# Optimization experiments

Hardware: AMD Instinct MI355X
Metric: run time of the kernel (lower is better)

The kernel has to match this reference:

```python
import jax, jax.numpy as jnp
import numpy as np

B, T, V, H = 256, 2048, 128, 64  # batch, seq_len, vocab/input_size, hidden_size


def setup_inputs() -> dict:
    key = jax.random.key(0)
    ks = jax.random.split(key, 11)
    s = 0.1  # weight scale
    d = jnp.float32
    return {
        "x": jax.random.normal(ks[0], (B, T, V), dtype=d),
        "W_f": jax.random.normal(ks[1], (V + H, H), dtype=d) * s,
        "b_f": jax.random.normal(ks[2], (H,), dtype=d) * s,
        "W_if": jax.random.normal(ks[3], (V + H, H), dtype=d) * s,
        "b_if": jax.random.normal(ks[4], (H,), dtype=d) * s,
        "W_ic": jax.random.normal(ks[5], (V + H, H), dtype=d) * s,
        "b_ic": jax.random.normal(ks[6], (H,), dtype=d) * s,
        "W_o": jax.random.normal(ks[7], (V + H, H), dtype=d) * s,
        "b_o": jax.random.normal(ks[8], (H,), dtype=d) * s,
        "W_out": jax.random.normal(ks[9], (H, V), dtype=d) * s,
        "b_out": jax.random.normal(ks[10], (V,), dtype=d) * s,
    }


def reference(x, W_f, b_f, W_if, b_if, W_ic, b_ic, W_o, b_o, W_out, b_out):
    # Manual LSTM cell from the source, stepped over time with lax.scan.
    # Per step (faithful to forward()+getOut()):
    #   s = concat(x_t, h);  f = sigmoid(s@W_f+b_f);  c = c*f
    #   add = tanh(s@W_ic+b_ic); af = sigmoid(s@W_if+b_if); c = c + add*af
    #   o = sigmoid(s@W_o+b_o);  h = tanh(c)*o
    #   out = softmax(h@W_out+b_out)
    b, t = x.shape[0], x.shape[1]
    h0 = jnp.zeros((b, W_f.shape[1]), dtype=x.dtype)
    c0 = jnp.zeros_like(h0)

    def step(carry, x_t):
        h, c = carry
        s = jnp.concatenate([x_t, h], axis=1)          # [B, V+H]
        f = jax.nn.sigmoid(s @ W_f + b_f)
        add = jnp.tanh(s @ W_ic + b_ic)
        af = jax.nn.sigmoid(s @ W_if + b_if)
        c = c * f + add * af
        o = jax.nn.sigmoid(s @ W_o + b_o)
        h = jnp.tanh(c) * o
        out = jax.nn.softmax(h @ W_out + b_out, axis=-1)  # [B, V]
        return (h, c), out

    (_, _), outs = jax.lax.scan(step, (h0, c0), jnp.swapaxes(x, 0, 1))
    return jnp.swapaxes(outs, 0, 1)  # [B, T, V]
```

## Files before the change

kernel.cpp:

```cpp
#include <hip/hip_runtime.h>
#include <cstdint>
#include <cstddef>

#define BB 256
#define TT 2048
#define VV 128
#define HH 64

typedef __attribute__((ext_vector_type(8))) short short8;
typedef __attribute__((ext_vector_type(4))) float f32x4;
typedef __attribute__((ext_vector_type(2))) float f32x2;

__device__ __forceinline__ float frcp(float x){ return __builtin_amdgcn_rcpf(x); }
__device__ __forceinline__ float sigm(float x){ return frcp(1.f + __expf(-x)); }
__device__ __forceinline__ float tanh_f(float x){ return 1.f - 2.f*frcp(1.f + __expf(2.f*x)); }

__device__ __forceinline__ void bar_lds(){
  asm volatile("s_waitcnt lgkmcnt(0)" ::: "memory");
  __builtin_amdgcn_s_barrier();
  __builtin_amdgcn_sched_barrier(0);
}

__device__ __forceinline__ void gload16(const void* g, void* l){
  __builtin_amdgcn_global_load_lds(
      (const __attribute__((address_space(1))) void*)g,
      (__attribute__((address_space(3))) void*)l, 16, 0, 0);
}

__device__ __forceinline__ unsigned short bf16hi(float x){
  unsigned u = __float_as_uint(x);
  return (unsigned short)((u + 0x7fffu + ((u>>16)&1u)) >> 16);
}
__device__ __forceinline__ void splitpack(const float* v8, short8& hi, short8& lo){
  #pragma unroll
  for (int j=0;j<8;++j){
    unsigned short h = bf16hi(v8[j]);
    float fh = __uint_as_float(((unsigned)h)<<16);
    unsigned short lw = bf16hi(v8[j] - fh);
    hi[j] = (short)h; lo[j] = (short)lw;
  }
}

__device__ __forceinline__ float qsum(float v){
  int t1 = __builtin_amdgcn_update_dpp(0, __float_as_int(v), 0xB1, 0xF, 0xF, true);
  v += __int_as_float(t1);
  int t2 = __builtin_amdgcn_update_dpp(0, __float_as_int(v), 0x4E, 0xF, 0xF, true);
  v += __int_as_float(t2);
  return v;
}

template<int CTRL>
__device__ __forceinline__ float dppmov(float v){
  return __int_as_float(__builtin_amdgcn_update_dpp(0, __float_as_int(v), CTRL, 0xF, 0xF, true));
}

__device__ __forceinline__ void pkfma(f32x2& acc, f32x2 a, f32x2 b){
  asm volatile("v_pk_fma_f32 %0, %1, %2, %0" : "+v"(acc) : "v"(a), "v"(b));
}

__global__ __launch_bounds__(256) void conv_w_k(
  const float* __restrict__ Wf, const float* __restrict__ Wi,
  const float* __restrict__ Wc, const float* __restrict__ Wo,
  const float* __restrict__ Wout,
  unsigned short* __restrict__ W4h, unsigned short* __restrict__ W4l,
  unsigned short* __restrict__ WOh, unsigned short* __restrict__ WOl)
{
  const int idx = blockIdx.x*256 + threadIdx.x;
  if (idx < 32768){
    const int j = idx&7, l=(idx>>3)&63, kk=(idx>>9)&3, nt=idx>>11;
    const int k = kk*32 + (l>>4)*8 + j;
    const int n = nt*16 + (l&15);
    const int g = n&3, colw = n>>2;
    const float* Ws = (g==0)?Wf:((g==1)?Wi:((g==2)?Wc:Wo));
    const float v = Ws[k*HH + colw];
    const unsigned short h = bf16hi(v);
    const float fh = __uint_as_float(((unsigned)h)<<16);
    W4h[idx] = h; W4l[idx] = bf16hi(v - fh);
  }
  if (idx < 8192){
    const int j = idx&7, l=(idx>>3)&63, kk=(idx>>9)&1, jt=idx>>10;
    const int k = kk*32 + (l>>4)*8 + j;
    const int jc = jt*16 + (l&15);
    const float v = Wout[k*VV + jc];
    const unsigned short h = bf16hi(v);
    const float fh = __uint_as_float(((unsigned)h)<<16);
    WOh[idx] = h; WOl[idx] = bf16hi(v - fh);
  }
}

__global__ __launch_bounds__(512,1) void pre_gemm_k(
  const float* __restrict__ x, const unsigned short* __restrict__ W4h,
  const unsigned short* __restrict__ W4l, float* __restrict__ PRE)
{
  __shared__ __align__(16) unsigned short XFh[16384];
  __shared__ __align__(16) unsigned short XFl[16384];
  const int tid = threadIdx.x, wv = tid>>6, l = tid&63, b = blockIdx.x;

  short8 Bh[2][4], Bl[2][4];
  #pragma unroll
  for (int ntl=0; ntl<2; ++ntl){
    const int nt = wv*2 + ntl;
    #pragma unroll
    for (int kk=0; kk<4; ++kk){
      Bh[ntl][kk] = *(const short8*)(W4h + ((nt*4+kk)*64 + l)*8);
      Bl[ntl][kk] = *(const short8*)(W4l + ((nt*4+kk)*64 + l)*8);
    }
  }

  #pragma unroll 1
  for (int mt=0; mt<16; ++mt){
    const size_t base_row = (size_t)b*TT + mt*128;
    #pragma unroll
    for (int i=0;i<4;++i){
      const int G = tid*4+i;
      const int lf = G&63, kk=(G>>6)&3, m8=G>>8;
      const float* src = x + (base_row + m8*16 + (lf&15))*VV + kk*32 + (lf>>4)*8;
      const f32x4 u = *(const f32x4*)src;
      const f32x4 v = *(const f32x4*)(src+4);
      float tmp[8] = {u[0],u[1],u[2],u[3], v[0],v[1],v[2],v[3]};
      short8 hi, lo; splitpack(tmp, hi, lo);
      *(short8*)&XFh[(size_t)G*8] = hi;
      *(short8*)&XFl[(size_t)G*8] = lo;
    }
    bar_lds();
    for (int m8=0; m8<8; ++m8){
      short8 Ah[4], Al[4];
      #pragma unroll
      for (int kk=0;kk<4;++kk){
        Ah[kk] = *(const short8*)&XFh[((m8*4+kk)*64 + l)*8];
        Al[kk] = *(const short8*)&XFl[((m8*4+kk)*64 + l)*8];
      }
      #pragma unroll
      for (int ntl=0; ntl<2; ++ntl){
        f32x4 acc = {0.f,0.f,0.f,0.f};
        #pragma unroll
        for (int kk=0;kk<4;++kk){
          acc = __builtin_amdgcn_mfma_f32_16x16x32_bf16(Al[kk], Bh[ntl][kk], acc, 0,0,0);
          acc = __builtin_amdgcn_mfma_f32_16x16x32_bf16(Ah[kk], Bl[ntl][kk], acc, 0,0,0);
          acc = __builtin_amdgcn_mfma_f32_16x16x32_bf16(Ah[kk], Bh[ntl][kk], acc, 0,0,0);
        }
        const int nt = wv*2 + ntl;
        float* dst = PRE + (base_row + m8*16 + (l>>4)*4)*256 + nt*16 + (l&15);
        #pragma unroll
        for (int r=0;r<4;++r) dst[(size_t)r*256] = acc[r];
      }
    }
    bar_lds();
  }
}

__global__ __launch_bounds__(256,1) void recur4_k(
  const float* __restrict__ W_f, const float* __restrict__ b_f,
  const float* __restrict__ W_if, const float* __restrict__ b_if,
  const float* __restrict__ W_ic, const float* __restrict__ b_ic,
  const float* __restrict__ W_o,  const float* __restrict__ b_o,
  const float* __restrict__ PRE,  float* __restrict__ H)
{
  __shared__ __align__(16) float ring[16*256];
  __shared__ __align__(16) float hring[32*HH];
  const int tid=threadIdx.x, wv=tid>>6, l=tid&63, b=blockIdx.x;
  const int col = wv*16 + (l>>2), q = l&3;
  const bool qb0 = (l&1)!=0, qb1 = (l&2)!=0;

  f32x2 wf2[8], wi2[8], wc2[8], wo2[8];
  #pragma unroll
  for (int m=0;m<8;++m){
    const size_t k0 = (size_t)(VV + q*16 + 2*m)*HH + col;
    wf2[m] = f32x2{W_f [k0], W_f [k0+HH]};
    wi2[m] = f32x2{W_if[k0], W_if[k0+HH]};
    wc2[m] = f32x2{W_ic[k0], W_ic[k0+HH]};
    wo2[m] = f32x2{W_o [k0], W_o [k0+HH]};
  }
  const float bq  = ((q==0)?b_f:(q==1)?b_if:(q==2)?b_ic:b_o)[col];
  const float sgn = (q==2)? 2.f : -1.f;
  const float aA  = (q==2)? -2.f : 1.f;
  const float aB  = (q==2)? 1.f : 0.f;

  const float* PREb = PRE + (size_t)b*TT*256;
  float* Hb = H + (size_t)b*TT*HH;
  const f32x4* ring4  = (const f32x4*)ring;
  const f32x4* hring4 = (const f32x4*)hring;

  if (tid < HH) hring[31*HH + tid] = 0.f;

  if (wv==0){
    asm volatile("s_waitcnt vmcnt(0)" ::: "memory");
    #pragma unroll 1
    for (int s=0;s<15;++s) gload16(PREb + s*256 + l*4, &ring[s*256]);
    asm volatile("s_waitcnt vmcnt(14)" ::: "memory");
  }
  bar_lds();

  float c_ = 0.f;
  #pragma unroll 1
  for (int t=0;t<TT;++t){
    if (wv==1 && t>0 && (t&15)==0){
      #pragma unroll
      for (int i=0;i<4;++i){
        const int rt = t-16 + i*4 + (l>>4);
        const f32x4 v = hring4[(rt&31)*16 + (l&15)];
        *(f32x4*)(Hb + (size_t)rt*HH + (l&15)*4) = v;
      }
    }
    const int rprev = (t+31)&31;
    const f32x4 pre = ring4[(t&15)*64 + col];
    const f32x4* hp = &hring4[rprev*16 + q*4];
    const f32x4 h0 = hp[0], h1 = hp[1], h2 = hp[2], h3 = hp[3];
    f32x2 a0={0.f,0.f}, a1={0.f,0.f}, a2={0.f,0.f}, a3={0.f,0.f};
    {
      const f32x2 p0 = f32x2{h0[0],h0[1]}, p1 = f32x2{h0[2],h0[3]};
      const f32x2 p2 = f32x2{h1[0],h1[1]}, p3 = f32x2{h1[2],h1[3]};
      const f32x2 p4 = f32x2{h2[0],h2[1]}, p5 = f32x2{h2[2],h2[3]};
      const f32x2 p6 = f32x2{h3[0],h3[1]}, p7 = f32x2{h3[2],h3[3]};
      pkfma(a0,p0,wf2[0]); pkfma(a0,p1,wf2[1]); pkfma(a0,p2,wf2[2]); pkfma(a0,p3,wf2[3]);
      pkfma(a0,p4,wf2[4]); pkfma(a0,p5,wf2[5]); pkfma(a0,p6,wf2[6]); pkfma(a0,p7,wf2[7]);
      pkfma(a1,p0,wi2[0]); pkfma(a1,p1,wi2[1]); pkfma(a1,p2,wi2[2]); pkfma(a1,p3,wi2[3]);
      pkfma(a1,p4,wi2[4]); pkfma(a1,p5,wi2[5]); pkfma(a1,p6,wi2[6]); pkfma(a1,p7,wi2[7]);
      pkfma(a2,p0,wc2[0]); pkfma(a2,p1,wc2[1]); pkfma(a2,p2,wc2[2]); pkfma(a2,p3,wc2[3]);
      pkfma(a2,p4,wc2[4]); pkfma(a2,p5,wc2[5]); pkfma(a2,p6,wc2[6]); pkfma(a2,p7,wc2[7]);
      pkfma(a3,p0,wo2[0]); pkfma(a3,p1,wo2[1]); pkfma(a3,p2,wo2[2]); pkfma(a3,p3,wo2[3]);
      pkfma(a3,p4,wo2[4]); pkfma(a3,p5,wo2[5]); pkfma(a3,p6,wo2[6]); pkfma(a3,p7,wo2[7]);
    }
    const float a0s = a0[0]+a0[1];
    const float a1s = a1[0]+a1[1];
    const float a2s = a2[0]+a2[1];
    const float a3s = a3[0]+a3[1];
    float tA = qb0 ? a1s : a0s;
    float tB = qb0 ? a0s : a1s;
    tA += dppmov<0xB1>(tB);
    float tC = qb0 ? a3s : a2s;
    float tD = qb0 ? a2s : a3s;
    tC += dppmov<0xB1>(tD);
    float r  = qb1 ? tC : tA;
    float rr = qb1 ? tA : tC;
    r += dppmov<0x4E>(rr);
    const float pm01 = qb0 ? pre[1] : pre[0];
    const float pm23 = qb0 ? pre[3] : pre[2];
    const float pq   = qb1 ? pm23 : pm01;
    const float xx  = r + pq + bq;
    const float e   = __expf(sgn*xx);
    const float rc  = frcp(1.f + e);
    const float act = fmaf(aA, rc, aB);
    const float f_  = dppmov<0x00>(act);
    const float af  = dppmov<0x55>(act);
    const float ad  = dppmov<0xAA>(act);
    const float o_  = dppmov<0xFF>(act);
    c_ = c_*f_ + ad*af;
    const float hv = tanh_f(c_) * o_;
    if (q==0) hring[(t&31)*HH + col] = hv;
    if (wv==0){
      gload16(PREb + (size_t)((t+15)&(TT-1))*256 + l*4, &ring[((t+15)&15)*256]);
      asm volatile("s_waitcnt vmcnt(14)" ::: "memory");
    }
    bar_lds();
  }
  if (wv==1){
    #pragma unroll
    for (int i=0;i<4;++i){
      const int rt = TT-16 + i*4 + (l>>4);
      const f32x4 v = hring4[(rt&31)*16 + (l&15)];
      *(f32x4*)(Hb + (size_t)rt*HH + (l&15)*4) = v;
    }
  }
}

__global__ __launch_bounds__(512,1) void logit_k(
  const float* __restrict__ H, const unsigned short* __restrict__ WOh,
  const unsigned short* __restrict__ WOl, const float* __restrict__ b_out,
  float* __restrict__ out)
{
  const int tid=threadIdx.x, wv=tid>>6, l=tid&63, b=blockIdx.x;
  short8 Bh[8][2], Bl[8][2];
  #pragma unroll
  for (int jt=0;jt<8;++jt){
    #pragma unroll
    for (int kk=0;kk<2;++kk){
      Bh[jt][kk] = *(const short8*)(WOh + ((jt*2+kk)*64 + l)*8);
      Bl[jt][kk] = *(const short8*)(WOl + ((jt*2+kk)*64 + l)*8);
    }
  }
  float bj[8];
  #pragma unroll
  for (int jt=0;jt<8;++jt) bj[jt] = b_out[jt*16 + (l&15)];

  #pragma unroll 1
  for (int mt=0; mt<16; ++mt){
    const size_t row0 = (size_t)b*TT + mt*128 + wv*16;
    const float* hbase = H + (row0 + (l&15))*HH;
    short8 Ah[2], Al[2];
    #pragma unroll
    for (int kk=0;kk<2;++kk){
      const float* s = hbase + kk*32 + (l>>4)*8;
      const f32x4 u = *(const f32x4*)s;
      const f32x4 v = *(const f32x4*)(s+4);
      float tmp[8] = {u[0],u[1],u[2],u[3], v[0],v[1],v[2],v[3]};
      splitpack(tmp, Ah[kk], Al[kk]);
    }
    f32x4 acc[8];
    #pragma unroll
    for (int jt=0;jt<8;++jt){
      f32x4 a = {0.f,0.f,0.f,0.f};
      #pragma unroll
      for (int kk=0;kk<2;++kk){
        a = __builtin_amdgcn_mfma_f32_16x16x32_bf16(Al[kk], Bh[jt][kk], a, 0,0,0);
        a = __builtin_amdgcn_mfma_f32_16x16x32_bf16(Ah[kk], Bl[jt][kk], a, 0,0,0);
        a = __builtin_amdgcn_mfma_f32_16x16x32_bf16(Ah[kk], Bh[jt][kk], a, 0,0,0);
      }
      acc[jt] = a;
    }
    #pragma unroll
    for (int r=0;r<4;++r){
      float z[8];
      #pragma unroll
      for (int jt=0;jt<8;++jt) z[jt] = acc[jt][r] + bj[jt];
      float mx = z[0];
      #pragma unroll
      for (int jt=1;jt<8;++jt) mx = fmaxf(mx, z[jt]);
      mx = fmaxf(mx, __shfl_xor(mx,1));
      mx = fmaxf(mx, __shfl_xor(mx,2));
      mx = fmaxf(mx, __shfl_xor(mx,4));
      mx = fmaxf(mx, __shfl_xor(mx,8));
      float sum = 0.f;
      #pragma unroll
      for (int jt=0;jt<8;++jt){ z[jt] = __expf(z[jt]-mx); sum += z[jt]; }
      sum += __shfl_xor(sum,1);
      sum += __shfl_xor(sum,2);
      sum += __shfl_xor(sum,4);
      sum += __shfl_xor(sum,8);
      const float rs = frcp(sum);
      float* op = out + (row0 + (l>>4)*4 + r)*VV + (l&15);
      #pragma unroll
      for (int jt=0;jt<8;++jt) op[jt*16] = z[jt]*rs;
    }
  }
}

#define XA_IDX(buf,kk,q,s) ((buf)*2048 + (((kk)*4+(q))*16+(s))*8)
#define HA_IDX(buf,kk,q,s) ((buf)*1024 + (((kk)*4+(q))*16+(s))*8)
#define NBF 128

__device__ __forceinline__ void gload16f(const float* g, float* l){
  __builtin_amdgcn_global_load_lds(
      (const __attribute__((address_space(1))) void*)g,
      (__attribute__((address_space(3))) void*)l, 16, 0, 0);
}

__global__ __launch_bounds__(512, 1) void fused_fb_k(
  const float* __restrict__ x,
  const float* __restrict__ W_f,  const float* __restrict__ b_f,
  const float* __restrict__ W_if, const float* __restrict__ b_if,
  const float* __restrict__ W_ic, const float* __restrict__ b_ic,
  const float* __restrict__ W_o,  const float* __restrict__ b_o,
  const float* __restrict__ W_out,const float* __restrict__ b_out,
  float* __restrict__ out)
{
  __shared__ __align__(16) float XR[4*16*VV];
  __shared__ __align__(16) short XAh[2*2048];
  __shared__ __align__(16) short XAl[2*2048];
  __shared__ __align__(16) float PRE[32*256];
  __shared__ __align__(16) short HAh[2*1024];
  __shared__ __align__(16) short HAl[2*1024];
  __shared__ __align__(16) float HR[32*HH];

  const int tid = threadIdx.x;
  const int wv  = tid >> 6;
  const int l   = tid & 63;
  const int row = blockIdx.x;
  const float* xrow = x   + (size_t)row*TT*VV;
  float*       orow = out + (size_t)row*TT*VV;

  if (wv < 4) {
    const int col = (wv&3)*16 + (l>>2);
    const int q   = l&3;
    float wh0[16], wh1[16], wh2[16], wh3[16];
    #pragma unroll
    for (int m=0;m<16;++m){
      const size_t kidx = (size_t)(VV + q*16 + m)*HH + col;
      wh0[m]=W_f[kidx]; wh1[m]=W_if[kidx]; wh2[m]=W_ic[kidx]; wh3[m]=W_o[kidx];
    }
    const float b0=b_f[col], b1=b_if[col], b2=b_ic[col], b3=b_o[col];
    if (tid < HH) HR[31*HH + tid] = 0.f;
    bar_lds(); bar_lds(); bar_lds();
    float c = 0.f;
    #pragma unroll 1
    for (int t=0; t<TT; ++t){
      const f32x4* hp = (const f32x4*)&HR[((t+31)&31)*HH + q*16];
      const f32x4 pre4 = *(const f32x4*)&PRE[(t&31)*256 + col*4];
      float d0=0.f,d1=0.f,d2=0.f,d3=0.f;
      #pragma unroll
      for (int m=0;m<4;++m){
        const f32x4 hv = hp[m];
        #pragma unroll
        for (int e=0;e<4;++e){
          const float s = hv[e];
          d0 = fmaf(s, wh0[m*4+e], d0);
          d1 = fmaf(s, wh1[m*4+e], d1);
          d2 = fmaf(s, wh2[m*4+e], d2);
          d3 = fmaf(s, wh3[m*4+e], d3);
        }
      }
      d0 = qsum(d0); d1 = qsum(d1); d2 = qsum(d2); d3 = qsum(d3);
      const float f  = sigm(d0 + pre4[0] + b0);
      const float fi = sigm(d1 + pre4[1] + b1);
      const float ci = tanh_f(d2 + pre4[2] + b2);
      const float o  = sigm(d3 + pre4[3] + b3);
      c = c*f + ci*fi;
      const float hv2 = tanh_f(c) * o;
      if (q==0) HR[(t&31)*HH + col] = hv2;
      bar_lds();
    }
    bar_lds();
  } else {
    const int pv = wv - 4;
    const int pt = pv*64 + l;
    short8 Bh[4][4], Bl[4][4];
    #pragma unroll
    for (int ntl=0; ntl<4; ++ntl){
      const int n = (pv*4+ntl)*16 + (l&15);
      const int g = n&3, colw = n>>2;
      const float* Ws = (g==0)?W_f:((g==1)?W_if:((g==2)?W_ic:W_o));
      #pragma unroll
      for (int kk=0;kk<4;++kk){
        float tmp[8];
        #pragma unroll
        for (int j=0;j<8;++j) tmp[j] = Ws[(size_t)(kk*32+(l>>4)*8+j)*HH + colw];
        splitpack(tmp, Bh[ntl][kk], Bl[ntl][kk]);
      }
    }
    short8 Lh[2][2], Ll[2][2];
    #pragma unroll
    for (int jt=0; jt<2; ++jt){
      const int j = (pv*2+jt)*16 + (l&15);
      #pragma unroll
      for (int kk=0;kk<2;++kk){
        float tmp[8];
        #pragma unroll
        for (int jj=0;jj<8;++jj) tmp[jj] = W_out[(size_t)(kk*32+(l>>4)*8+jj)*VV + j];
        splitpack(tmp, Lh[jt][kk], Ll[jt][kk]);
      }
    }
    auto GLOAD = [&](int bb){
      #pragma unroll
      for (int i=0;i<2;++i){
        const float* src = xrow + (size_t)bb*16*VV + pv*512 + i*256 + l*4;
        float* dst = &XR[(bb&3)*2048 + pv*512 + i*256];
        gload16f(src, dst);
      }
    };
    auto CONV = [&](int bb){
      if (pt < 256){
        const int buf=bb&1, kk=pt>>6, qq=(pt>>4)&3, s=pt&15;
        const float* src = &XR[(bb&3)*2048 + s*VV + kk*32 + qq*8];
        float tmp[8];
        #pragma unroll
        for (int j=0;j<8;++j) tmp[j] = src[j];
        short8 hi, lo; splitpack(tmp, hi, lo);
        *(short8*)&XAh[XA_IDX(buf,kk,qq,s)] = hi;
        *(short8*)&XAl[XA_IDX(buf,kk,qq,s)] = lo;
      }
    };
    auto PREB = [&](int bb){
      const int buf = bb&1;
      short8 Ah[4], Al[4];
      #pragma unroll
      for (int kk=0;kk<4;++kk){
        Ah[kk] = *(const short8*)&XAh[XA_IDX(buf,kk,(l>>4),(l&15))];
        Al[kk] = *(const short8*)&XAl[XA_IDX(buf,kk,(l>>4),(l&15))];
      }
      #pragma unroll
      for (int ntl=0; ntl<4; ++ntl){
        f32x4 acc = {0.f,0.f,0.f,0.f};
        #pragma unroll
        for (int kk=0;kk<4;++kk){
          acc = __builtin_amdgcn_mfma_f32_16x16x32_bf16(Al[kk], Bh[ntl][kk], acc, 0,0,0);
          acc = __builtin_amdgcn_mfma_f32_16x16x32_bf16(Ah[kk], Bl[ntl][kk], acc, 0,0,0);
          acc = __builtin_amdgcn_mfma_f32_16x16x32_bf16(Ah[kk], Bh[ntl][kk], acc, 0,0,0);
        }
        const int n  = (pv*4+ntl)*16 + (l&15);
        const int s0 = buf*16 + (l>>4)*4;
        #pragma unroll
        for (int r=0;r<4;++r) PRE[(s0+r)*256 + n] = acc[r];
      }
    };
    auto LOGB = [&](int bb){
      const int buf = bb&1;
      short8 Ah[2], Al[2];
      #pragma unroll
      for (int kk=0;kk<2;++kk){
        Ah[kk] = *(const short8*)&HAh[HA_IDX(buf,kk,(l>>4),(l&15))];
        Al[kk] = *(const short8*)&HAl[HA_IDX(buf,kk,(l>>4),(l&15))];
      }
      #pragma unroll
      for (int jt=0; jt<2; ++jt){
        f32x4 acc = {0.f,0.f,0.f,0.f};
        #pragma unroll
        for (int kk=0;kk<2;++kk){
          acc = __builtin_amdgcn_mfma_f32_16x16x32_bf16(Al[kk], Lh[jt][kk], acc, 0,0,0);
          acc = __builtin_amdgcn_mfma_f32_16x16x32_bf16(Ah[kk], Ll[jt][kk], acc, 0,0,0);
          acc = __builtin_amdgcn_mfma_f32_16x16x32_bf16(Ah[kk], Lh[jt][kk], acc, 0,0,0);
        }
        const int j  = (pv*2+jt)*16 + (l&15);
        const int t0 = bb*16 + (l>>4)*4;
        #pragma unroll
        for (int r=0;r<4;++r) orow[(size_t)(t0+r)*VV + j] = acc[r];
      }
    };
    auto RELAY = [&](int hs2){
      if (pt < 8){
        const int kk = pt>>2, qq = pt&3;
        const int buf = (hs2>>4)&1, s = hs2&15;
        const float* src = &HR[(hs2&31)*HH + kk*32 + qq*8];
        float tmp[8];
        #pragma unroll
        for (int j=0;j<8;++j) tmp[j] = src[j];
        short8 hi, lo; splitpack(tmp, hi, lo);
        *(short8*)&HAh[HA_IDX(buf,kk,qq,s)] = hi;
        *(short8*)&HAl[HA_IDX(buf,kk,qq,s)] = lo;
      }
    };
    GLOAD(0); GLOAD(1); GLOAD(2);
    asm volatile("s_waitcnt vmcnt(2)" ::: "memory");
    bar_lds();
    CONV(0); CONV(1);
    bar_lds();
    PREB(0);
    bar_lds();
    #pragma unroll 1
    for (int t=0; t<TT; ++t){
      if (t >= 1) RELAY(t-1);
      const int slot = t&15, blk = t>>4;
      if (slot==0){ if (blk+1 < NBF) PREB(blk+1); }
      else if (slot==1){ if (blk >= 1) LOGB(blk-1); }
      else if (slot==2){ if (blk+3 < NBF) GLOAD(blk+3); }
      else if (slot==3){ if (blk+2 < NBF) asm volatile("s_waitcnt vmcnt(2)" ::: "memory"); }
      else if (slot==4){ if (blk+2 < NBF) CONV(blk+2); }
      bar_lds();
    }
    RELAY(TT-1);
    bar_lds();
    LOGB(NBF-1);
  }
}

__global__ __launch_bounds__(256) void softmax_fb_k(float* __restrict__ out)
{
  const int r = blockIdx.x*4 + (threadIdx.x>>6);
  const int l = threadIdx.x & 63;
  float2* p = (float2*)(out + (size_t)r*VV);
  float2 v = p[l];
  float m = fmaxf(v.x, v.y);
  #pragma unroll
  for (int d=1; d<64; d<<=1) m = fmaxf(m, __shfl_xor(m, d));
  float e0 = __expf(v.x - m), e1 = __expf(v.y - m);
  float s = e0 + e1;
  #pragma unroll
  for (int d=1; d<64; d<<=1) s += __shfl_xor(s, d);
  float rs = frcp(s);
  p[l] = make_float2(e0*rs, e1*rs);
}

extern "C" void kernel_launch(void* const* d_in, const int* in_sizes, int n_in,
                              void* d_out, int out_size, void* d_ws, size_t ws_size,
                              hipStream_t stream) {
  const float* x     = (const float*)d_in[0];
  const float* W_f   = (const float*)d_in[1];
  const float* b_f   = (const float*)d_in[2];
  const float* W_if  = (const float*)d_in[3];
  const float* b_if  = (const float*)d_in[4];
  const float* W_ic  = (const float*)d_in[5];
  const float* b_ic  = (const float*)d_in[6];
  const float* W_o   = (const float*)d_in[7];
  const float* b_o   = (const float*)d_in[8];
  const float* W_out = (const float*)d_in[9];
  const float* b_out = (const float*)d_in[10];
  float* out = (float*)d_out;

  const size_t PRE_B = (size_t)BB*TT*256*sizeof(float);
  const size_t H_B   = (size_t)BB*TT*HH*sizeof(float);
  const size_t need  = PRE_B + H_B + 2*32768*2 + 2*8192*2;

  if (ws_size >= need) {
    char* w = (char*)d_ws;
    float* PRE  = (float*)w;
    float* Hbuf = (float*)(w + PRE_B);
    unsigned short* W4h = (unsigned short*)(w + PRE_B + H_B);
    unsigned short* W4l = W4h + 32768;
    unsigned short* WOh = W4l + 32768;
    unsigned short* WOl = WOh + 8192;
    hipLaunchKernelGGL(conv_w_k, dim3(128), dim3(256), 0, stream,
                       W_f, W_if, W_ic, W_o, W_out, W4h, W4l, WOh, WOl);
    hipLaunchKernelGGL(pre_gemm_k, dim3(BB), dim3(512), 0, stream, x, W4h, W4l, PRE);
    hipLaunchKernelGGL(recur4_k, dim3(BB), dim3(256), 0, stream,
                       W_f, b_f, W_if, b_if, W_ic, b_ic, W_o, b_o, PRE, Hbuf);
    hipLaunchKernelGGL(logit_k, dim3(BB), dim3(512), 0, stream, Hbuf, WOh, WOl, b_out, out);
  } else {
    hipLaunchKernelGGL(fused_fb_k, dim3(BB), dim3(512), 0, stream,
                       x, W_f, b_f, W_if, b_if, W_ic, b_ic, W_o, b_o,
                       W_out, b_out, out);
    hipLaunchKernelGGL(softmax_fb_k, dim3(BB*TT/4), dim3(256), 0, stream, out);
  }
}
```

Measured before the change: 990.9 us.

## Prefetch recurrence pre-activations into registers instead of an LDS ring

The recurrence kernel no longer has wave 0 stream pre-activation rows into an LDS ring with global_load_lds and explicit vmcnt waits. Each thread now loads its own single pre-activation value straight from global memory into a register array, eight timesteps ahead. The time loop is unrolled by 8 with incrementally updated ring offsets. This removes the per-step LDS read of pre-activations and wave 0's serialized load-and-wait from the critical path. In exchange, every thread issues its own global load each step, and latency hiding now depends on how the compiler places vmcnt waits, which the interleaved H stores may disturb.

```diff
diff --git a/kernel.cpp b/kernel.cpp
--- a/kernel.cpp
+++ b/kernel.cpp
@@ -149,14 +149,13 @@
   }
 }
 
-__global__ __launch_bounds__(256,1) void recur4_k(
+__global__ __launch_bounds__(256,1) void recur8_k(
   const float* __restrict__ W_f, const float* __restrict__ b_f,
   const float* __restrict__ W_if, const float* __restrict__ b_if,
   const float* __restrict__ W_ic, const float* __restrict__ b_ic,
   const float* __restrict__ W_o,  const float* __restrict__ b_o,
   const float* __restrict__ PRE,  float* __restrict__ H)
 {
-  __shared__ __align__(16) float ring[16*256];
   __shared__ __align__(16) float hring[32*HH];
   const int tid=threadIdx.x, wv=tid>>6, l=tid&63, b=blockIdx.x;
   const int col = wv*16 + (l>>2), q = l&3;
@@ -176,83 +175,83 @@
   const float aA  = (q==2)? -2.f : 1.f;
   const float aB  = (q==2)? 1.f : 0.f;
 
-  const float* PREb = PRE + (size_t)b*TT*256;
+  const float* PREl = PRE + (size_t)b*TT*256 + wv*64 + l;
   float* Hb = H + (size_t)b*TT*HH;
-  const f32x4* ring4  = (const f32x4*)ring;
   const f32x4* hring4 = (const f32x4*)hring;
 
   if (tid < HH) hring[31*HH + tid] = 0.f;
 
-  if (wv==0){
-    asm volatile("s_waitcnt vmcnt(0)" ::: "memory");
-    #pragma unroll 1
-    for (int s=0;s<15;++s) gload16(PREb + s*256 + l*4, &ring[s*256]);
-    asm volatile("s_waitcnt vmcnt(14)" ::: "memory");
-  }
+  float pf[8];
+  #pragma unroll
+  for (int j=0;j<8;++j) pf[j] = PREl[(size_t)j*256];
+
   bar_lds();
 
   float c_ = 0.f;
+  int hoff = 31*16 + q*4;
+  int woff = col;
+
   #pragma unroll 1
-  for (int t=0;t<TT;++t){
-    if (wv==1 && t>0 && (t&15)==0){
-      #pragma unroll
-      for (int i=0;i<4;++i){
-        const int rt = t-16 + i*4 + (l>>4);
-        const f32x4 v = hring4[(rt&31)*16 + (l&15)];
-        *(f32x4*)(Hb + (size_t)rt*HH + (l&15)*4) = v;
-      }
-    }
-    const int rprev = (t+31)&31;
-    const f32x4 pre = ring4[(t&15)*64 + col];
-    const f32x4* hp = &hring4[rprev*16 + q*4];
-    const f32x4 h0 = hp[0], h1 = hp[1], h2 = hp[2], h3 = hp[3];
-    f32x2 a0={0.f,0.f}, a1={0.f,0.f}, a2={0.f,0.f}, a3={0.f,0.f};
-    {
-      const f32x2 p0 = f32x2{h0[0],h0[1]}, p1 = f32x2{h0[2],h0[3]};
-      const f32x2 p2 = f32x2{h1[0],h1[1]}, p3 = f32x2{h1[2],h1[3]};
-      const f32x2 p4 = f32x2{h2[0],h2[1]}, p5 = f32x2{h2[2],h2[3]};
-      const f32x2 p6 = f32x2{h3[0],h3[1]}, p7 = f32x2{h3[2],h3[3]};
-      pkfma(a0,p0,wf2[0]); pkfma(a0,p1,wf2[1]); pkfma(a0,p2,wf2[2]); pkfma(a0,p3,wf2[3]);
-      pkfma(a0,p4,wf2[4]); pkfma(a0,p5,wf2[5]); pkfma(a0,p6,wf2[6]); pkfma(a0,p7,wf2[7]);
-      pkfma(a1,p0,wi2[0]); pkfma(a1,p1,wi2[1]); pkfma(a1,p2,wi2[2]); pkfma(a1,p3,wi2[3]);
-      pkfma(a1,p4,wi2[4]); pkfma(a1,p5,wi2[5]); pkfma(a1,p6,wi2[6]); pkfma(a1,p7,wi2[7]);
-      pkfma(a2,p0,wc2[0]); pkfma(a2,p1,wc2[1]); pkfma(a2,p2,wc2[2]); pkfma(a2,p3,wc2[3]);
-      pkfma(a2,p4,wc2[4]); pkfma(a2,p5,wc2[5]); pkfma(a2,p6,wc2[6]); pkfma(a2,p7,wc2[7]);
-      pkfma(a3,p0,wo2[0]); pkfma(a3,p1,wo2[1]); pkfma(a3,p2,wo2[2]); pkfma(a3,p3,wo2[3]);
-      pkfma(a3,p4,wo2[4]); pkfma(a3,p5,wo2[5]); pkfma(a3,p6,wo2[6]); pkfma(a3,p7,wo2[7]);
-    }
-    const float a0s = a0[0]+a0[1];
-    const float a1s = a1[0]+a1[1];
-    const float a2s = a2[0]+a2[1];
-    const float a3s = a3[0]+a3[1];
-    float tA = qb0 ? a1s : a0s;
-    float tB = qb0 ? a0s : a1s;
-    tA += dppmov<0xB1>(tB);
-    float tC = qb0 ? a3s : a2s;
-    float tD = qb0 ? a2s : a3s;
-    tC += dppmov<0xB1>(tD);
-    float r  = qb1 ? tC : tA;
-    float rr = qb1 ? tA : tC;
-    r += dppmov<0x4E>(rr);
-    const float pm01 = qb0 ? pre[1] : pre[0];
-    const float pm23 = qb0 ? pre[3] : pre[2];
-    const float pq   = qb1 ? pm23 : pm01;
-    const float xx  = r + pq + bq;
-    const float e   = __expf(sgn*xx);
-    const float rc  = frcp(1.f + e);
-    const float act = fmaf(aA, rc, aB);
-    const float f_  = dppmov<0x00>(act);
-    const float af  = dppmov<0x55>(act);
-    const float ad  = dppmov<0xAA>(act);
-    const float o_  = dppmov<0xFF>(act);
-    c_ = c_*f_ + ad*af;
-    const float hv = tanh_f(c_) * o_;
-    if (q==0) hring[(t&31)*HH + col] = hv;
-    if (wv==0){
-      gload16(PREb + (size_t)((t+15)&(TT-1))*256 + l*4, &ring[((t+15)&15)*256]);
-      asm volatile("s_waitcnt vmcnt(14)" ::: "memory");
-    }
-    bar_lds();
+  for (int t8=0; t8<TT; t8+=8){
+    #pragma unroll
+    for (int j=0;j<8;++j){
+      const int t = t8+j;
+      if (wv==1 && t>0 && (t&15)==0){
+        #pragma unroll
+        for (int i=0;i<4;++i){
+          const int rt = t-16 + i*4 + (l>>4);
+          const f32x4 v = hring4[(rt&31)*16 + (l&15)];
+          *(f32x4*)(Hb + (size_t)rt*HH + (l&15)*4) = v;
+        }
+      }
+      const f32x4 h0 = hring4[hoff+0], h1 = hring4[hoff+1];
+      const f32x4 h2 = hring4[hoff+2], h3 = hring4[hoff+3];
+      const float nxt = PREl[(size_t)((t+8)&(TT-1))*256];
+      const float pq = pf[j];
+      f32x2 a0={0.f,0.f}, a1={0.f,0.f}, a2={0.f,0.f}, a3={0.f,0.f};
+      {
+        const f32x2 p0 = f32x2{h0[0],h0[1]}, p1 = f32x2{h0[2],h0[3]};
+        const f32x2 p2 = f32x2{h1[0],h1[1]}, p3 = f32x2{h1[2],h1[3]};
+        const f32x2 p4 = f32x2{h2[0],h2[1]}, p5 = f32x2{h2[2],h2[3]};
+        const f32x2 p6 = f32x2{h3[0],h3[1]}, p7 = f32x2{h3[2],h3[3]};
+        pkfma(a0,p0,wf2[0]); pkfma(a0,p1,wf2[1]); pkfma(a0,p2,wf2[2]); pkfma(a0,p3,wf2[3]);
+        pkfma(a0,p4,wf2[4]); pkfma(a0,p5,wf2[5]); pkfma(a0,p6,wf2[6]); pkfma(a0,p7,wf2[7]);
+        pkfma(a1,p0,wi2[0]); pkfma(a1,p1,wi2[1]); pkfma(a1,p2,wi2[2]); pkfma(a1,p3,wi2[3]);
+        pkfma(a1,p4,wi2[4]); pkfma(a1,p5,wi2[5]); pkfma(a1,p6,wi2[6]); pkfma(a1,p7,wi2[7]);
+        pkfma(a2,p0,wc2[0]); pkfma(a2,p1,wc2[1]); pkfma(a2,p2,wc2[2]); pkfma(a2,p3,wc2[3]);
+        pkfma(a2,p4,wc2[4]); pkfma(a2,p5,wc2[5]); pkfma(a2,p6,wc2[6]); pkfma(a2,p7,wc2[7]);
+        pkfma(a3,p0,wo2[0]); pkfma(a3,p1,wo2[1]); pkfma(a3,p2,wo2[2]); pkfma(a3,p3,wo2[3]);
+        pkfma(a3,p4,wo2[4]); pkfma(a3,p5,wo2[5]); pkfma(a3,p6,wo2[6]); pkfma(a3,p7,wo2[7]);
+      }
+      const float a0s = a0[0]+a0[1];
+      const float a1s = a1[0]+a1[1];
+      const float a2s = a2[0]+a2[1];
+      const float a3s = a3[0]+a3[1];
+      float tA = qb0 ? a1s : a0s;
+      float tB = qb0 ? a0s : a1s;
+      tA += dppmov<0xB1>(tB);
+      float tC = qb0 ? a3s : a2s;
+      float tD = qb0 ? a2s : a3s;
+      tC += dppmov<0xB1>(tD);
+      float r  = qb1 ? tC : tA;
+      float rr = qb1 ? tA : tC;
+      r += dppmov<0x4E>(rr);
+      const float xx  = r + pq + bq;
+      const float e   = __expf(sgn*xx);
+      const float rc  = frcp(1.f + e);
+      const float act = fmaf(aA, rc, aB);
+      const float f_  = dppmov<0x00>(act);
+      const float af  = dppmov<0x55>(act);
+      const float ad  = dppmov<0xAA>(act);
+      const float o_  = dppmov<0xFF>(act);
+      c_ = c_*f_ + ad*af;
+      const float hv = tanh_f(c_) * o_;
+      if (q==0) hring[woff] = hv;
+      pf[j] = nxt;
+      hoff = (hoff + 16) & 511;
+      woff = (woff + 64) & 2047;
+      bar_lds();
+    }
   }
   if (wv==1){
     #pragma unroll
@@ -590,7 +589,7 @@
     hipLaunchKernelGGL(conv_w_k, dim3(128), dim3(256), 0, stream,
                        W_f, W_if, W_ic, W_o, W_out, W4h, W4l, WOh, WOl);
     hipLaunchKernelGGL(pre_gemm_k, dim3(BB), dim3(512), 0, stream, x, W4h, W4l, PRE);
-    hipLaunchKernelGGL(recur4_k, dim3(BB), dim3(256), 0, stream,
+    hipLaunchKernelGGL(recur8_k, dim3(BB), dim3(256), 0, stream,
                        W_f, b_f, W_if, b_if, W_ic, b_ic, W_o, b_o, PRE, Hbuf);
     hipLaunchKernelGGL(logit_k, dim3(BB), dim3(512), 0, stream, Hbuf, WOh, WOl, b_out, out);
   } else {
```

Measured after the change: 905.7 us. 1.09x faster.
